# Performance work log

Measured on AMD Instinct MI355X. Metric: run time of the kernel, lower is better.

Reference implementation:

```python
import jax, jax.numpy as jnp
import numpy as np

RADIUS = 1.3
COARSE = 64
FINE = 2
N_ATOMS = 64
SH_DIM = 9
DATA_DIM = SH_DIM * 3 + 1  # 28
N_INTRS = COARSE * 3 * 2 * FINE  # 768
STEP = (RADIUS * 2.0 / COARSE / FINE) / 2.0
BATCH = 1024


def sh_basis(d):
    # real spherical harmonics basis, degree 2 (9 coeffs), on normalized dirs
    d = d / jnp.linalg.norm(d, axis=-1, keepdims=True)
    x, y, z = d[..., 0], d[..., 1], d[..., 2]
    C0 = 0.28209479177387814
    C1 = 0.4886025119029199
    C20, C21, C22, C23, C24 = (1.0925484305920792, -1.0925484305920792,
                               0.31539156525252005, -1.0925484305920792,
                               0.5462742152960396)
    return jnp.stack([
        C0 * jnp.ones_like(x), -C1 * y, C1 * z, -C1 * x,
        C20 * x * y, C21 * y * z, C22 * (2.0 * z * z - x * x - y * y),
        C23 * x * z, C24 * (x * x - y * y)
    ], axis=-1)


def dict_interp(grid, atoms, pts):
    # l2_interp_v2: coarse-voxel dictionary coeffs x trilinear fine-atom interp
    # pts: [P,3] in [0,1)
    P = pts.shape[0]
    pc = pts * COARSE
    c = jnp.clip(jnp.floor(pc), 0, COARSE - 1).astype(jnp.int32)
    local = pc - c.astype(pts.dtype)  # position inside coarse voxel, [0,1)
    clin = (c[:, 0] * COARSE + c[:, 1]) * COARSE + c[:, 2]
    coeff = grid[clin]                              # [P, A]
    # project dictionary coeffs through atoms for every fine cell: [P, FINE^3, D]
    proj = jnp.einsum('pa,fad->pfd', coeff, atoms)
    u = local * FINE - 0.5
    f = jnp.floor(u)
    t = u - f
    i0 = jnp.clip(f, 0, FINE - 1).astype(jnp.int32)
    i1 = jnp.clip(f + 1.0, 0, FINE - 1).astype(jnp.int32)
    idx = jnp.stack([i0, i1], axis=-1)              # [P,3,2]
    w = jnp.stack([1.0 - t, t], axis=-1)            # [P,3,2]
    rows = jnp.arange(P)
    out = jnp.zeros((P, DATA_DIM), dtype=pts.dtype)
    for kx in (0, 1):
        for ky in (0, 1):
            for kz in (0, 1):
                lin = (idx[:, 0, kx] * FINE + idx[:, 1, ky]) * FINE + idx[:, 2, kz]
                wgt = w[:, 0, kx] * w[:, 1, ky] * w[:, 2, kz]
                out = out + wgt[:, None] * proj[rows, lin]
    return out


def _forward(rays_o, rays_d, grid, atoms):
    dt = rays_o.dtype
    # ---- sample_proposal (no grad) ----
    off_pos = (RADIUS - rays_o) / rays_d
    off_neg = (-RADIUS - rays_o) / rays_d
    start = jnp.max(jnp.minimum(off_pos, off_neg), axis=-1, keepdims=True)
    intersections = jax.lax.stop_gradient(
        start + jnp.arange(N_INTRS, dtype=dt)[None, :] * STEP)  # [B, 768]
    tr = intersections[:, :-1]  # [B, 767]
    pts = rays_o[:, None, :] + tr[..., None] * rays_d[:, None, :]  # [B,n,3]
    mask = jnp.all((pts > -RADIUS) & (pts < RADIUS), axis=-1)      # [B,n]
    pts = jax.lax.stop_gradient(pts)
    B, n = tr.shape
    # normalized coords in [0,1); masked-out points are clipped then zeroed later
    p = jnp.clip((pts + RADIUS) / (2.0 * RADIUS), 0.0, 1.0 - 1e-6).reshape(-1, 3)
    data = dict_interp(grid, atoms, p).reshape(B, n, DATA_DIM)
    # masked_scatter of sigma <=> dense compute + where(mask, ., 0)
    sigma = jnp.where(mask, jax.nn.relu(data[..., -1]), 0.0)
    dists = (intersections[:, 1:] - intersections[:, :-1]) * \
        jnp.linalg.norm(rays_d, axis=-1, keepdims=True)
    alpha = 1.0 - jnp.exp(-sigma * dists)
    trans = jnp.cumprod(1.0 - alpha + 1e-10, axis=-1)
    trans = jnp.concatenate([jnp.ones_like(trans[:, :1]), trans[:, :-1]], axis=-1)
    abs_light = alpha * trans  # per-sample weights
    sh_mult = sh_basis(rays_d)                      # [B, 9]
    sh = data[..., :-1].reshape(B, n, 3, SH_DIM)
    rgb_samp = jnp.einsum('bnck,bk->bnc', sh, sh_mult)
    rgb_samp = jax.nn.sigmoid(jnp.where(mask[..., None], rgb_samp, 0.0))
    comp = jnp.sum(abs_light[..., None] * rgb_samp, axis=1)  # [B,3]
    acc = jnp.sum(abs_light, axis=1)
    rgb = comp + (1.0 - acc)[:, None]  # white background
    depth = jnp.sum(abs_light * tr, axis=1)
    return rgb, alpha, depth


def setup_inputs():
    key = jax.random.key(0)
    k0, k1, k2, k3 = jax.random.split(key, 4)
    o = jax.random.normal(k0, (BATCH, 3), dtype=jnp.float32)
    o = o / jnp.linalg.norm(o, axis=-1, keepdims=True) * 2.5
    d = -o + 0.3 * jax.random.normal(k1, (BATCH, 3), dtype=jnp.float32)
    d = d / jnp.linalg.norm(d, axis=-1, keepdims=True)
    grid = 0.01 * jax.random.normal(k2, (COARSE ** 3, N_ATOMS), dtype=jnp.float32)
    atoms_sh = jax.random.uniform(k3, (FINE ** 3, N_ATOMS, DATA_DIM - 1), dtype=jnp.float32)
    atoms = jnp.concatenate(
        [atoms_sh, jnp.full((FINE ** 3, N_ATOMS, 1), 0.01, dtype=jnp.float32)], axis=-1)
    return {"rays_o": o, "rays_d": d, "grid": grid, "atoms": atoms, "grid_id": 0}


def reference(rays_o, rays_d, grid, atoms, grid_id):
    # grid_id selects among num_scenes grids; num_scenes=1 so grid is pre-selected
    return _forward(rays_o, rays_d, grid, atoms)
```

## Files before the change

kernel.cpp:

```cpp
#include <hip/hip_runtime.h>
#include <hip/hip_bf16.h>

#define RADIUS_F 1.3f
#define NSAMP 767
#define STEPF 0.01015625f
#define BATCH 1024

typedef __attribute__((ext_vector_type(8))) short short8;
typedef __attribute__((ext_vector_type(4))) float floatx4;
typedef __fp16 fp16x2 __attribute__((ext_vector_type(2)));

static __device__ __forceinline__ unsigned pkbf(float a, float b) {
    union { __hip_bfloat162 h; unsigned u; } cvt;
    cvt.h = __float22bfloat162_rn(make_float2(a, b));
    return cvt.u;
}
static __device__ __forceinline__ unsigned pkh(float a, float b) {
    union { fp16x2 h; unsigned u; } c;
    c.h = __builtin_amdgcn_cvt_pkrtz(a, b);
    return c.u;
}
static __device__ __forceinline__ float2 uph(unsigned u) {
    union { unsigned u; fp16x2 h; } c; c.u = u;
    return make_float2((float)c.h.x, (float)c.h.y);
}
static __device__ __forceinline__ float bfhi(unsigned u) {
    union { unsigned u; float f; } c; c.u = u << 16; return c.f;
}

static __device__ __forceinline__ float coset4_sum(float p) {
    int q4 = __builtin_amdgcn_update_dpp(0, __float_as_int(p), 0x124, 0xf, 0xf, true);
    p = p + __int_as_float(q4);
    int q8 = __builtin_amdgcn_update_dpp(0, __float_as_int(p), 0x128, 0xf, 0xf, true);
    return p + __int_as_float(q8);
}

__launch_bounds__(512, 8)
__global__ void plenoxels_fwd(const float* __restrict__ rays_o,
                              const float* __restrict__ rays_d,
                              const float* __restrict__ grid,
                              const float* __restrict__ atoms,
                              float* __restrict__ out)
{
    __shared__ __align__(16) __hip_bfloat16 BpL[32 * 64];
    __shared__ unsigned WpU[768 * 5];
    __shared__ __align__(4) __hip_bfloat16 alphaL[768];
    __shared__ __align__(4) __hip_bfloat16 rgbL[768 * 3];
    __shared__ float wprodL[8];
    __shared__ float partL[8][5];

    const int tid  = threadIdx.x;
    const int ray  = blockIdx.x;
    const int lane = tid & 63;
    const int w    = tid >> 6;
    const int m    = lane & 15;
    const int quad = lane >> 4;

    const float ox = rays_o[ray * 3 + 0], oy = rays_o[ray * 3 + 1], oz = rays_o[ray * 3 + 2];
    const float dx = rays_d[ray * 3 + 0], dy = rays_d[ray * 3 + 1], dz = rays_d[ray * 3 + 2];

    float start;
    {
        float a0 = (RADIUS_F - ox) / dx, b0 = (-RADIUS_F - ox) / dx;
        float a1 = (RADIUS_F - oy) / dy, b1 = (-RADIUS_F - oy) / dy;
        float a2 = (RADIUS_F - oz) / dz, b2 = (-RADIUS_F - oz) / dz;
        start = fmaxf(fminf(a0, b0), fmaxf(fminf(a1, b1), fminf(a2, b2)));
    }
    const float dnorm = sqrtf(dx * dx + dy * dy + dz * dz);
    const float dist = STEPF * dnorm;

    auto geom = [&](int s) -> int {
        float tr = start + (float)s * STEPF;
        float px = ox + tr * dx, py = oy + tr * dy, pz = oz + tr * dz;
        int mask = (px > -RADIUS_F) & (px < RADIUS_F) &
                   (py > -RADIUS_F) & (py < RADIUS_F) &
                   (pz > -RADIUS_F) & (pz < RADIUS_F) & (s < NSAMP);
        float maskf = mask ? 1.f : 0.f;
        const float sc = 1.0f / (2.0f * RADIUS_F);
        float qx = fminf(fmaxf((px + RADIUS_F) * sc, 0.f), 1.0f - 1e-6f);
        float qy = fminf(fmaxf((py + RADIUS_F) * sc, 0.f), 1.0f - 1e-6f);
        float qz = fminf(fmaxf((pz + RADIUS_F) * sc, 0.f), 1.0f - 1e-6f);
        float pcx = qx * 64.f, pcy = qy * 64.f, pcz = qz * 64.f;
        float cx = fminf(floorf(pcx), 63.f);
        float cy = fminf(floorf(pcy), 63.f);
        float cz = fminf(floorf(pcz), 63.f);
        float lx = pcx - cx, ly = pcy - cy, lz = pcz - cz;
        int clin = (((int)cx * 64) + (int)cy) * 64 + (int)cz;
        float xw0, xw1, yw0, yw1, zw0, zw1;
        {
            float u = lx * 2.f - 0.5f, fF = floorf(u), t = u - fF;
            xw0 = (fF < 0.f) ? 1.f : ((fF > 0.f) ? 0.f : 1.f - t);
            xw1 = (fF < 0.f) ? 0.f : ((fF > 0.f) ? 1.f : t);
        }
        {
            float u = ly * 2.f - 0.5f, fF = floorf(u), t = u - fF;
            yw0 = (fF < 0.f) ? 1.f : ((fF > 0.f) ? 0.f : 1.f - t);
            yw1 = (fF < 0.f) ? 0.f : ((fF > 0.f) ? 1.f : t);
        }
        {
            float u = lz * 2.f - 0.5f, fF = floorf(u), t = u - fF;
            zw0 = (fF < 0.f) ? 1.f : ((fF > 0.f) ? 0.f : 1.f - t);
            zw1 = (fF < 0.f) ? 0.f : ((fF > 0.f) ? 1.f : t);
        }
        xw0 *= maskf; xw1 *= maskf;
        float g0 = yw0 * zw0, g1 = yw0 * zw1, g2 = yw1 * zw0, g3 = yw1 * zw1;
        unsigned* wr = &WpU[s * 5];
        wr[0] = pkh(xw0 * g0, xw1 * g0);
        wr[1] = pkh(xw0 * g1, xw1 * g1);
        wr[2] = pkh(xw0 * g2, xw1 * g2);
        wr[3] = pkh(xw0 * g3, xw1 * g3);
        return clin;
    };

    int clinA = geom(w * 96 + lane);
    int clinB = 0;
    if (lane < 32) clinB = geom(w * 96 + 64 + lane);

    const float4* g4 = (const float4*)grid;
    float4 cv0, cv1, cv2, cv3;
    {
        int clinC = __shfl(clinA, m, 64);
        const float4* gp = g4 + (clinC << 4) + (quad << 2);
        cv0 = gp[0]; cv1 = gp[1]; cv2 = gp[2]; cv3 = gp[3];
    }

    {
        float shm[9];
        float inv = 1.0f / dnorm;
        float nx = dx * inv, ny = dy * inv, nz = dz * inv;
        shm[0] = 0.28209479177387814f;
        shm[1] = -0.4886025119029199f * ny;
        shm[2] = 0.4886025119029199f * nz;
        shm[3] = -0.4886025119029199f * nx;
        shm[4] = 1.0925484305920792f * nx * ny;
        shm[5] = -1.0925484305920792f * ny * nz;
        shm[6] = 0.31539156525252005f * (2.f * nz * nz - nx * nx - ny * ny);
        shm[7] = -1.0925484305920792f * nx * nz;
        shm[8] = 0.5462742152960396f * (nx * nx - ny * ny);
        for (int idx = tid; idx < 2048; idx += 512) {
            int col = idx >> 6, a = idx & 63;
            int f = col >> 2, c = col & 3;
            const float* base = atoms + (f * 64 + a) * 28;
            float sv;
            if (c == 3) sv = base[27];
            else {
                sv = 0.f;
                #pragma unroll
                for (int i = 0; i < 9; ++i) sv = fmaf(base[c * 9 + i], shm[i], sv);
            }
            BpL[col * 64 + a] = __float2bfloat16(sv);
        }
    }
    __syncthreads();

    short8 bq00, bq01, bq10, bq11;
    {
        const short* bs = (const short*)BpL;
        const short* p0 = bs + m * 64 + (quad << 4);
        bq00 = *(const short8*)(p0);
        bq01 = *(const short8*)(p0 + 8);
        const short* p1 = bs + (16 + m) * 64 + (quad << 4);
        bq10 = *(const short8*)(p1);
        bq11 = *(const short8*)(p1 + 8);
    }

    float* out_rgb   = out;
    float* out_alpha = out + BATCH * 3;
    float* out_depth = out + BATCH * 3 + BATCH * NSAMP;
    const int f0 = m >> 2;

    #pragma unroll
    for (int t = 0; t < 6; ++t) {
        union { unsigned u[4]; short8 s; } a0, a1;
        a0.u[0] = pkbf(cv0.x, cv0.y); a0.u[1] = pkbf(cv0.z, cv0.w);
        a0.u[2] = pkbf(cv1.x, cv1.y); a0.u[3] = pkbf(cv1.z, cv1.w);
        a1.u[0] = pkbf(cv2.x, cv2.y); a1.u[1] = pkbf(cv2.z, cv2.w);
        a1.u[2] = pkbf(cv3.x, cv3.y); a1.u[3] = pkbf(cv3.z, cv3.w);

        if (t < 5) {
            int tn = t + 1;
            int clinC = (tn < 4) ? __shfl(clinA, (tn << 4) + m, 64)
                                 : __shfl(clinB, ((tn - 4) << 4) + m, 64);
            const float4* gp = g4 + (clinC << 4) + (quad << 2);
            cv0 = gp[0]; cv1 = gp[1]; cv2 = gp[2]; cv3 = gp[3];
        }

        floatx4 acc0 = {0.f, 0.f, 0.f, 0.f};
        floatx4 acc1 = {0.f, 0.f, 0.f, 0.f};
        acc0 = __builtin_amdgcn_mfma_f32_16x16x32_bf16(a0.s, bq00, acc0, 0, 0, 0);
        acc0 = __builtin_amdgcn_mfma_f32_16x16x32_bf16(a1.s, bq01, acc0, 0, 0, 0);
        acc1 = __builtin_amdgcn_mfma_f32_16x16x32_bf16(a0.s, bq10, acc1, 0, 0, 0);
        acc1 = __builtin_amdgcn_mfma_f32_16x16x32_bf16(a1.s, bq11, acc1, 0, 0, 0);

        #pragma unroll
        for (int r = 0; r < 4; ++r) {
            int s = w * 96 + (t << 4) + (quad << 2) + r;
            float2 wab = uph(WpU[s * 5 + f0]);
            float p = wab.x * acc0[r] + wab.y * acc1[r];
            p = coset4_sum(p);
            if (m == 3) {
                float al = 1.f - __expf(-fmaxf(p, 0.f) * dist);
                if (s < NSAMP) out_alpha[ray * NSAMP + s] = al;
                alphaL[s] = __float2bfloat16(al);
            } else if (m < 3) {
                rgbL[s * 3 + m] = __float2bfloat16(1.f / (1.f + __expf(-p)));
            }
        }
    }

    __syncthreads();

    {
        const bool act = (tid < 384);
        const int s0 = tid * 2;
        float a0 = 0.f, a1 = 0.f;
        if (act) {
            unsigned aa = *(const unsigned*)&alphaL[s0];
            a0 = bfhi(aa & 0xffff);
            a1 = bfhi(aa >> 16);
        }
        float pr = (1.f - a0 + 1e-10f) * (1.f - a1 + 1e-10f);

        float incl = pr;
        #pragma unroll
        for (int off = 1; off < 64; off <<= 1) {
            float v = __shfl_up(incl, off, 64);
            if (lane >= off) incl *= v;
        }
        if (lane == 63) wprodL[w] = incl;
        __syncthreads();

        float base = 1.f;
        #pragma unroll
        for (int ww = 0; ww < 5; ++ww)
            if (w > ww) base *= wprodL[ww];
        float excl = __shfl_up(incl, 1, 64);
        if (lane == 0) excl = 1.f;
        float trans = base * excl;

        float c0 = 0.f, c1 = 0.f, c2 = 0.f, accw = 0.f, dep = 0.f;
        if (act) {
            unsigned u01 = *(const unsigned*)&rgbL[s0 * 3];
            unsigned u23 = *(const unsigned*)&rgbL[s0 * 3 + 2];
            unsigned u45 = *(const unsigned*)&rgbL[s0 * 3 + 4];
            float w0 = a0 * trans;
            c0 += w0 * bfhi(u01 & 0xffff);
            c1 += w0 * bfhi(u01 >> 16);
            c2 += w0 * bfhi(u23 & 0xffff);
            accw += w0;
            dep += w0 * (start + (float)s0 * STEPF);
            trans *= (1.f - a0 + 1e-10f);
            float w1 = a1 * trans;
            c0 += w1 * bfhi(u23 >> 16);
            c1 += w1 * bfhi(u45 & 0xffff);
            c2 += w1 * bfhi(u45 >> 16);
            accw += w1;
            dep += w1 * (start + (float)(s0 + 1) * STEPF);
        }
        #pragma unroll
        for (int off = 1; off < 64; off <<= 1) {
            c0   += __shfl_xor(c0, off, 64);
            c1   += __shfl_xor(c1, off, 64);
            c2   += __shfl_xor(c2, off, 64);
            accw += __shfl_xor(accw, off, 64);
            dep  += __shfl_xor(dep, off, 64);
        }
        if (lane == 0) {
            partL[w][0] = c0; partL[w][1] = c1; partL[w][2] = c2;
            partL[w][3] = accw; partL[w][4] = dep;
        }
        __syncthreads();
        if (tid == 0) {
            float C0 = 0.f, C1 = 0.f, C2 = 0.f, AC = 0.f, DP = 0.f;
            #pragma unroll
            for (int ww = 0; ww < 6; ++ww) {
                C0 += partL[ww][0]; C1 += partL[ww][1]; C2 += partL[ww][2];
                AC += partL[ww][3]; DP += partL[ww][4];
            }
            float bg = 1.f - AC;
            out_rgb[ray * 3 + 0] = C0 + bg;
            out_rgb[ray * 3 + 1] = C1 + bg;
            out_rgb[ray * 3 + 2] = C2 + bg;
            out_depth[ray] = DP;
        }
    }
}

extern "C" void kernel_launch(void* const* d_in, const int* in_sizes, int n_in,
                              void* d_out, int out_size, void* d_ws, size_t ws_size,
                              hipStream_t stream) {
    const float* rays_o = (const float*)d_in[0];
    const float* rays_d = (const float*)d_in[1];
    const float* grid   = (const float*)d_in[2];
    const float* atoms  = (const float*)d_in[3];
    float* out = (float*)d_out;
    hipLaunchKernelGGL(plenoxels_fwd, dim3(BATCH), dim3(512), 0, stream,
                       rays_o, rays_d, grid, atoms, out);
}
```

Before: 121.9 us.

## Vectorize atom projection and defer alpha/sigmoid activation to compositing stage

The atom/SH projection becomes one thread per (fine cell, atom) row with seven float4 loads, replacing the strided loop of scalar loads. The MFMA stage now stores raw pre-activation values into a single packed 4-channel bf16 LDS array. The exp, sigmoid and alpha global store move into the compositing stage, which reads all channels for two samples with one 16-byte LDS load. This cuts divergent lane work in the MFMA loop and the number of LDS transactions. In exchange, alpha is now computed from a bf16-rounded density, which changes the precision of the alpha output, and the alpha stores are strided per thread rather than contiguous.

```diff
diff --git a/kernel.cpp b/kernel.cpp
--- a/kernel.cpp
+++ b/kernel.cpp
@@ -24,8 +24,8 @@
     union { unsigned u; fp16x2 h; } c; c.u = u;
     return make_float2((float)c.h.x, (float)c.h.y);
 }
-static __device__ __forceinline__ float bfhi(unsigned u) {
-    union { unsigned u; float f; } c; c.u = u << 16; return c.f;
+static __device__ __forceinline__ float bfx(unsigned short u) {
+    union { unsigned u; float f; } c; c.u = ((unsigned)u) << 16; return c.f;
 }
 
 static __device__ __forceinline__ float coset4_sum(float p) {
@@ -44,8 +44,7 @@
 {
     __shared__ __align__(16) __hip_bfloat16 BpL[32 * 64];
     __shared__ unsigned WpU[768 * 5];
-    __shared__ __align__(4) __hip_bfloat16 alphaL[768];
-    __shared__ __align__(4) __hip_bfloat16 rgbL[768 * 3];
+    __shared__ __align__(16) __hip_bfloat16 pL[768 * 4];
     __shared__ float wprodL[8];
     __shared__ float partL[8][5];
 
@@ -137,19 +136,29 @@
         shm[6] = 0.31539156525252005f * (2.f * nz * nz - nx * nx - ny * ny);
         shm[7] = -1.0925484305920792f * nx * nz;
         shm[8] = 0.5462742152960396f * (nx * nx - ny * ny);
-        for (int idx = tid; idx < 2048; idx += 512) {
-            int col = idx >> 6, a = idx & 63;
-            int f = col >> 2, c = col & 3;
-            const float* base = atoms + (f * 64 + a) * 28;
-            float sv;
-            if (c == 3) sv = base[27];
-            else {
-                sv = 0.f;
-                #pragma unroll
-                for (int i = 0; i < 9; ++i) sv = fmaf(base[c * 9 + i], shm[i], sv);
-            }
-            BpL[col * 64 + a] = __float2bfloat16(sv);
-        }
+
+        const float* base = atoms + tid * 28;
+        float4 v0 = *(const float4*)(base);
+        float4 v1 = *(const float4*)(base + 4);
+        float4 v2 = *(const float4*)(base + 8);
+        float4 v3 = *(const float4*)(base + 12);
+        float4 v4 = *(const float4*)(base + 16);
+        float4 v5 = *(const float4*)(base + 20);
+        float4 v6 = *(const float4*)(base + 24);
+
+        float s0 = v0.x*shm[0] + v0.y*shm[1] + v0.z*shm[2] + v0.w*shm[3]
+                 + v1.x*shm[4] + v1.y*shm[5] + v1.z*shm[6] + v1.w*shm[7] + v2.x*shm[8];
+        float s1 = v2.y*shm[0] + v2.z*shm[1] + v2.w*shm[2] + v3.x*shm[3]
+                 + v3.y*shm[4] + v3.z*shm[5] + v3.w*shm[6] + v4.x*shm[7] + v4.y*shm[8];
+        float s2 = v4.z*shm[0] + v4.w*shm[1] + v5.x*shm[2] + v5.y*shm[3]
+                 + v5.z*shm[4] + v5.w*shm[5] + v6.x*shm[6] + v6.y*shm[7] + v6.z*shm[8];
+
+        int f = tid >> 6, a = tid & 63;
+        int cb = (f << 2) << 6;
+        BpL[cb + a]        = __float2bfloat16(s0);
+        BpL[cb + 64 + a]   = __float2bfloat16(s1);
+        BpL[cb + 128 + a]  = __float2bfloat16(s2);
+        BpL[cb + 192 + a]  = __float2bfloat16(v6.w);
     }
     __syncthreads();
 
@@ -198,13 +207,7 @@
             float2 wab = uph(WpU[s * 5 + f0]);
             float p = wab.x * acc0[r] + wab.y * acc1[r];
             p = coset4_sum(p);
-            if (m == 3) {
-                float al = 1.f - __expf(-fmaxf(p, 0.f) * dist);
-                if (s < NSAMP) out_alpha[ray * NSAMP + s] = al;
-                alphaL[s] = __float2bfloat16(al);
-            } else if (m < 3) {
-                rgbL[s * 3 + m] = __float2bfloat16(1.f / (1.f + __expf(-p)));
-            }
+            if (m < 4) pL[(s << 2) + m] = __float2bfloat16(p);
         }
     }
 
@@ -214,10 +217,19 @@
         const bool act = (tid < 384);
         const int s0 = tid * 2;
         float a0 = 0.f, a1 = 0.f;
+        float r0 = 0.f, g0 = 0.f, b0 = 0.f, r1 = 0.f, g1 = 0.f, b1 = 0.f;
         if (act) {
-            unsigned aa = *(const unsigned*)&alphaL[s0];
-            a0 = bfhi(aa & 0xffff);
-            a1 = bfhi(aa >> 16);
+            short8 pv = *(const short8*)&pL[s0 << 2];
+            a0 = 1.f - __expf(-fmaxf(bfx((unsigned short)pv[3]), 0.f) * dist);
+            a1 = 1.f - __expf(-fmaxf(bfx((unsigned short)pv[7]), 0.f) * dist);
+            r0 = 1.f / (1.f + __expf(-bfx((unsigned short)pv[0])));
+            g0 = 1.f / (1.f + __expf(-bfx((unsigned short)pv[1])));
+            b0 = 1.f / (1.f + __expf(-bfx((unsigned short)pv[2])));
+            r1 = 1.f / (1.f + __expf(-bfx((unsigned short)pv[4])));
+            g1 = 1.f / (1.f + __expf(-bfx((unsigned short)pv[5])));
+            b1 = 1.f / (1.f + __expf(-bfx((unsigned short)pv[6])));
+            out_alpha[ray * NSAMP + s0] = a0;
+            if (s0 + 1 < NSAMP) out_alpha[ray * NSAMP + s0 + 1] = a1;
         }
         float pr = (1.f - a0 + 1e-10f) * (1.f - a1 + 1e-10f);
 
@@ -240,20 +252,13 @@
 
         float c0 = 0.f, c1 = 0.f, c2 = 0.f, accw = 0.f, dep = 0.f;
         if (act) {
-            unsigned u01 = *(const unsigned*)&rgbL[s0 * 3];
-            unsigned u23 = *(const unsigned*)&rgbL[s0 * 3 + 2];
-            unsigned u45 = *(const unsigned*)&rgbL[s0 * 3 + 4];
             float w0 = a0 * trans;
-            c0 += w0 * bfhi(u01 & 0xffff);
-            c1 += w0 * bfhi(u01 >> 16);
-            c2 += w0 * bfhi(u23 & 0xffff);
+            c0 += w0 * r0; c1 += w0 * g0; c2 += w0 * b0;
             accw += w0;
             dep += w0 * (start + (float)s0 * STEPF);
             trans *= (1.f - a0 + 1e-10f);
             float w1 = a1 * trans;
-            c0 += w1 * bfhi(u23 >> 16);
-            c1 += w1 * bfhi(u45 & 0xffff);
-            c2 += w1 * bfhi(u45 >> 16);
+            c0 += w1 * r1; c1 += w1 * g1; c2 += w1 * b1;
             accw += w1;
             dep += w1 * (start + (float)(s0 + 1) * STEPF);
         }
```

Result: faster. 114.7 us (-6.0%).
